# Kernel tuning notes

Hardware: AMD Instinct MI355X
Metric: run time of the kernel (lower is better)

Reference implementation:

```python
import jax, jax.numpy as jnp
import numpy as np

DIM = 512
HEADS = 16
GRID = (32, 32)
MLP_HIDDEN = 2048
EPS = 1e-5


def _relative_position_index(hw):
    H, W = hw
    coords = np.stack(np.meshgrid(np.arange(H), np.arange(W), indexing='ij'))  # [2,H,W]
    coords = coords.reshape(2, -1)  # [2, L]
    rel = coords[:, :, None] - coords[:, None, :]  # [2, L, L]
    rel = rel.transpose(1, 2, 0).astype(np.int64)  # [L, L, 2]
    rel[:, :, 0] += H - 1
    rel[:, :, 1] += W - 1
    rel[:, :, 0] *= 2 * W - 1
    return jnp.asarray(rel.sum(-1))  # [L, L]


def setup_inputs() -> dict:
    key = jax.random.key(0)
    ks = jax.random.split(key, 12)
    L = GRID[0] * GRID[1]
    table_size = (2 * GRID[0] - 1) * (2 * GRID[1] - 1)
    s = 0.02
    return {
        'x': jax.random.normal(ks[0], (8, L, DIM), jnp.float32),
        'rel_index': _relative_position_index(GRID),
        'bias_table': s * jax.random.truncated_normal(ks[1], -2.0, 2.0, (table_size, HEADS), jnp.float32),
        'qkv_w': jax.random.normal(ks[2], (DIM, 3 * DIM), jnp.float32) / np.sqrt(DIM),
        'qkv_b': jnp.zeros((3 * DIM,), jnp.float32),
        'proj_w': jax.random.normal(ks[3], (DIM, DIM), jnp.float32) / np.sqrt(DIM),
        'proj_b': jnp.zeros((DIM,), jnp.float32),
        'n1_g': jnp.ones((DIM,), jnp.float32),
        'n1_b': jnp.zeros((DIM,), jnp.float32),
        'n2_g': jnp.ones((DIM,), jnp.float32),
        'n2_b': jnp.zeros((DIM,), jnp.float32),
        'fc1_w': jax.random.normal(ks[4], (DIM, MLP_HIDDEN), jnp.float32) / np.sqrt(DIM),
        'fc1_b': jnp.zeros((MLP_HIDDEN,), jnp.float32),
        'fc2_w': jax.random.normal(ks[5], (MLP_HIDDEN, DIM), jnp.float32) / np.sqrt(MLP_HIDDEN),
        'fc2_b': jnp.zeros((DIM,), jnp.float32),
    }


def _layernorm(x, g, b):
    mu = jnp.mean(x, -1, keepdims=True)
    var = jnp.mean(jnp.square(x - mu), -1, keepdims=True)
    return (x - mu) * jax.lax.rsqrt(var + EPS) * g + b


def reference(x, rel_index, bias_table, qkv_w, qkv_b, proj_w, proj_b,
              n1_g, n1_b, n2_g, n2_b, fc1_w, fc1_b, fc2_w, fc2_b):
    B, L, C = x.shape
    hd = C // HEADS
    scale = hd ** -0.5

    h = _layernorm(x, n1_g, n1_b)
    qkv = (h @ qkv_w + qkv_b).reshape(B, L, 3, HEADS, hd)
    qkv = jnp.transpose(qkv, (2, 0, 3, 1, 4))  # [3, B, H, L, hd]
    q, k, v = qkv[0] * scale, qkv[1], qkv[2]

    attn = jnp.einsum('bhld,bhmd->bhlm', q, k)  # [B, H, L, L]
    bias = bias_table[rel_index]                # [L, L, H]
    attn = attn + jnp.transpose(bias, (2, 0, 1))[None]
    attn = jax.nn.softmax(attn, axis=-1)

    out = jnp.einsum('bhlm,bhmd->bhld', attn, v)
    out = jnp.transpose(out, (0, 2, 1, 3)).reshape(B, L, C)
    out = out @ proj_w + proj_b

    x = x + out
    h2 = _layernorm(x, n2_g, n2_b)
    mlp = jax.nn.gelu(h2 @ fc1_w + fc1_b, approximate=False) @ fc2_w + fc2_b
    return x + mlp
```

## Files before the change

kernel.cpp:

```cpp
#include <hip/hip_runtime.h>

typedef unsigned short u16;
typedef __attribute__((ext_vector_type(8))) short bf16x8;
typedef __attribute__((ext_vector_type(4))) float f32x4;

__device__ __forceinline__ float bf2f(unsigned int u) {
    union { unsigned int i; float f; } c; c.i = u << 16; return c.f;
}
__device__ __forceinline__ unsigned int f2bf(float f) {
    union { float f; unsigned int i; } c; c.f = f;
    unsigned int x = c.i;
    unsigned int r = x + 0x7FFFu + ((x >> 16) & 1u);
    return r >> 16;
}

__device__ __forceinline__ void gload_lds16(const u16* g, u16* l) {
    __builtin_amdgcn_global_load_lds(
        (__attribute__((address_space(1))) void*)const_cast<u16*>(g),
        (__attribute__((address_space(3))) void*)l,
        16, 0, 0);
}

__global__ __launch_bounds__(256) void wconv_kernel(const float* __restrict__ W,
                                                    u16* __restrict__ Wt, int K, int N) {
    __shared__ u16 tile[32][36];
    int k0 = blockIdx.y * 32, n0 = blockIdx.x * 32;
    int t = threadIdx.x;
    int r = t >> 3, c4 = (t & 7) * 4;
    float4 v = *(const float4*)(W + (size_t)(k0 + r) * N + n0 + c4);
    tile[r][c4 + 0] = (u16)f2bf(v.x);
    tile[r][c4 + 1] = (u16)f2bf(v.y);
    tile[r][c4 + 2] = (u16)f2bf(v.z);
    tile[r][c4 + 3] = (u16)f2bf(v.w);
    __syncthreads();
    int n = t >> 3, k4 = (t & 7) * 4;
    u16 a0 = tile[k4 + 0][n], a1 = tile[k4 + 1][n];
    u16 a2 = tile[k4 + 2][n], a3 = tile[k4 + 3][n];
    uint2 st;
    st.x = (unsigned)a0 | ((unsigned)a1 << 16);
    st.y = (unsigned)a2 | ((unsigned)a3 << 16);
    *(uint2*)(Wt + (size_t)(n0 + n) * K + k0 + k4) = st;
}

__global__ __launch_bounds__(256) void ln_kernel(const float* __restrict__ x,
                                                 const float* __restrict__ g,
                                                 const float* __restrict__ b,
                                                 u16* __restrict__ y) {
    int row = blockIdx.x * 4 + (threadIdx.x >> 6);
    int t = threadIdx.x & 63;
    const float* xr = x + (size_t)row * 512 + t * 8;
    float4 a = *(const float4*)xr;
    float4 c = *(const float4*)(xr + 4);
    float v[8] = { a.x, a.y, a.z, a.w, c.x, c.y, c.z, c.w };
    float s = 0.f, ss = 0.f;
#pragma unroll
    for (int i = 0; i < 8; ++i) { s += v[i]; ss += v[i] * v[i]; }
#pragma unroll
    for (int off = 32; off; off >>= 1) {
        s  += __shfl_down(s, off);
        ss += __shfl_down(ss, off);
    }
    s = __shfl(s, 0); ss = __shfl(ss, 0);
    float mu = s * (1.0f / 512.0f);
    float var = ss * (1.0f / 512.0f) - mu * mu;
    float r = rsqrtf(var + 1e-5f);
    float4 g0 = *(const float4*)(g + t * 8);
    float4 g1 = *(const float4*)(g + t * 8 + 4);
    float4 b0 = *(const float4*)(b + t * 8);
    float4 b1 = *(const float4*)(b + t * 8 + 4);
    float gv[8] = { g0.x, g0.y, g0.z, g0.w, g1.x, g1.y, g1.z, g1.w };
    float bv[8] = { b0.x, b0.y, b0.z, b0.w, b1.x, b1.y, b1.z, b1.w };
    unsigned int o[4];
#pragma unroll
    for (int i = 0; i < 4; ++i) {
        float o0 = (v[2 * i] - mu) * r * gv[2 * i] + bv[2 * i];
        float o1 = (v[2 * i + 1] - mu) * r * gv[2 * i + 1] + bv[2 * i + 1];
        o[i] = f2bf(o0) | (f2bf(o1) << 16);
    }
    *(uint4*)(y + (size_t)row * 512 + t * 8) = make_uint4(o[0], o[1], o[2], o[3]);
}

template <int ACT, int RES, int COUT>
__global__ __launch_bounds__(256) void gemm_mfma(const u16* __restrict__ A, int lda,
                                                 const u16* __restrict__ Bt,
                                                 const float* __restrict__ bias,
                                                 const float* __restrict__ res, int ldres,
                                                 void* __restrict__ C, int ldC, int K) {
    __shared__ u16 As[2][64 * 32];
    __shared__ u16 Bs[2][128 * 32];
    int tid = threadIdx.x;
    int bm = blockIdx.y * 64, bn = blockIdx.x * 128;
    int lane = tid & 63, wv = tid >> 6;
    int q = lane >> 4, lr = lane & 15;
    int wr = wv >> 1, wc = wv & 1;

    const u16* Ag = A + (size_t)(bm + wv * 16 + (lane >> 2)) * lda + (lane & 3) * 8;
    const u16* Bg = Bt + (size_t)(bn + wv * 32 + (lane >> 2)) * K + (lane & 3) * 8;
    int aoff  = (wv * 16) * 32;
    int boff0 = (wv * 32) * 32;
    int boff1 = (wv * 32 + 16) * 32;
    int apf = (wr * 32 + lr) * 32 + q * 8;
    int bpf = (wc * 64 + lr) * 32 + q * 8;

    f32x4 acc[2][4];
#pragma unroll
    for (int i = 0; i < 2; ++i)
#pragma unroll
        for (int j = 0; j < 4; ++j) acc[i][j] = (f32x4){0.f, 0.f, 0.f, 0.f};

    gload_lds16(Ag, &As[0][aoff]);
    gload_lds16(Bg, &Bs[0][boff0]);
    gload_lds16(Bg + (size_t)16 * K, &Bs[0][boff1]);
    __syncthreads();

    int cur = 0;
    for (int k0 = 0; k0 < K; k0 += 32) {
        int nxt = cur ^ 1;
        if (k0 + 32 < K) {
            gload_lds16(Ag + k0 + 32, &As[nxt][aoff]);
            gload_lds16(Bg + k0 + 32, &Bs[nxt][boff0]);
            gload_lds16(Bg + (size_t)16 * K + k0 + 32, &Bs[nxt][boff1]);
        }
        bf16x8 af[2], bfr[4];
#pragma unroll
        for (int i = 0; i < 2; ++i) af[i] = *(const bf16x8*)&As[cur][apf + i * 16 * 32];
#pragma unroll
        for (int j = 0; j < 4; ++j) bfr[j] = *(const bf16x8*)&Bs[cur][bpf + j * 16 * 32];
#pragma unroll
        for (int i = 0; i < 2; ++i)
#pragma unroll
            for (int j = 0; j < 4; ++j)
                acc[i][j] = __builtin_amdgcn_mfma_f32_16x16x32_bf16(af[i], bfr[j], acc[i][j], 0, 0, 0);
        __syncthreads();
        cur = nxt;
    }

    float bv[4];
#pragma unroll
    for (int j = 0; j < 4; ++j)
        bv[j] = bias ? bias[bn + wc * 64 + j * 16 + lr] : 0.f;
#pragma unroll
    for (int i = 0; i < 2; ++i) {
#pragma unroll
        for (int j = 0; j < 4; ++j) {
            int col = bn + wc * 64 + j * 16 + lr;
#pragma unroll
            for (int r = 0; r < 4; ++r) {
                int row = bm + wr * 32 + i * 16 + q * 4 + r;
                float v = acc[i][j][r] + bv[j];
                if (ACT) v = 0.5f * v * (1.0f + erff(v * 0.7071067811865475f));
                if (RES) v += res[(size_t)row * ldres + col];
                if (COUT == 0) ((u16*)C)[(size_t)row * ldC + col] = (u16)f2bf(v);
                else           ((float*)C)[(size_t)row * ldC + col] = v;
            }
        }
    }
}

__global__ __launch_bounds__(256) void attn_mfma(u16* __restrict__ qkv,
                                                 const float* __restrict__ bias_table) {
    __shared__ u16 Ks[128][40];
    __shared__ u16 Vt[32][136];
    __shared__ u16 Ps[4][16][136];
    __shared__ float biasc[3969];
    int tid = threadIdx.x;
    int qt = blockIdx.x, h = blockIdx.y, z = blockIdx.z;
    u16* qkvz = qkv + (size_t)z * 1024 * 1536;

    for (int i = tid; i < 3969; i += 256) biasc[i] = bias_table[(size_t)i * 16 + h];

    int lane = tid & 63, wv = tid >> 6;
    int q = lane >> 4, m = lane & 15;

    int qrow = qt * 64 + wv * 16 + m;
    bf16x8 qf = *(const bf16x8*)(qkvz + (size_t)qrow * 1536 + h * 32 + q * 8);

    int arow[4];
#pragma unroll
    for (int r = 0; r < 4; ++r) {
        int l = qt * 64 + wv * 16 + q * 4 + r;
        arow[r] = (l >> 5) * 63 + (l & 31) + 1984;
    }

    const float scale = 0.17677669529663687f;
    float mrow[4] = { -1e30f, -1e30f, -1e30f, -1e30f };
    float lrow[4] = { 0.f, 0.f, 0.f, 0.f };
    f32x4 acco[2] = { (f32x4){0.f,0.f,0.f,0.f}, (f32x4){0.f,0.f,0.f,0.f} };

    int key = tid >> 1, dh = (tid & 1) * 16;
    const u16* kvsrc = qkvz + (size_t)key * 1536 + 512 + h * 32 + dh;
    uint4 pk0, pk1, pv0, pv1;
    pk0 = *(const uint4*)(kvsrc);
    pk1 = *(const uint4*)(kvsrc + 8);
    pv0 = *(const uint4*)(kvsrc + 512);
    pv1 = *(const uint4*)(kvsrc + 520);

    for (int kt = 0; kt < 8; ++kt) {
        __syncthreads();
        *(uint4*)&Ks[key][dh] = pk0;
        *(uint4*)&Ks[key][dh + 8] = pk1;
        {
            u16 tmp[16];
            *(uint4*)tmp = pv0; *(uint4*)(tmp + 8) = pv1;
#pragma unroll
            for (int j = 0; j < 16; ++j) Vt[dh + j][key] = tmp[j];
        }
        __syncthreads();
        if (kt < 7) {
            const u16* src = kvsrc + (size_t)(kt + 1) * 128 * 1536;
            pk0 = *(const uint4*)(src);
            pk1 = *(const uint4*)(src + 8);
            pv0 = *(const uint4*)(src + 512);
            pv1 = *(const uint4*)(src + 520);
        }

        f32x4 s8[8];
#pragma unroll
        for (int t = 0; t < 8; ++t) {
            bf16x8 kf = *(const bf16x8*)&Ks[t * 16 + m][q * 8];
            s8[t] = __builtin_amdgcn_mfma_f32_16x16x32_bf16(
                qf, kf, (f32x4){0.f,0.f,0.f,0.f}, 0, 0, 0);
        }
#pragma unroll
        for (int t = 0; t < 8; ++t) {
            int bb = (kt * 4 + (t >> 1)) * 63 + (t & 1) * 16 + m;
#pragma unroll
            for (int r = 0; r < 4; ++r)
                s8[t][r] = s8[t][r] * scale + biasc[arow[r] - bb];
        }
        float alpha[4];
#pragma unroll
        for (int r = 0; r < 4; ++r) {
            float v = s8[0][r];
#pragma unroll
            for (int t = 1; t < 8; ++t) v = fmaxf(v, s8[t][r]);
            v = fmaxf(v, __shfl_xor(v, 1));
            v = fmaxf(v, __shfl_xor(v, 2));
            v = fmaxf(v, __shfl_xor(v, 4));
            v = fmaxf(v, __shfl_xor(v, 8));
            float mn = fmaxf(mrow[r], v);
            alpha[r] = __expf(mrow[r] - mn);
            mrow[r] = mn;
            float sum = 0.f;
#pragma unroll
            for (int t = 0; t < 8; ++t) {
                float p = __expf(s8[t][r] - mn);
                s8[t][r] = p;
                sum += p;
            }
            sum += __shfl_xor(sum, 1);
            sum += __shfl_xor(sum, 2);
            sum += __shfl_xor(sum, 4);
            sum += __shfl_xor(sum, 8);
            lrow[r] = lrow[r] * alpha[r] + sum;
        }
#pragma unroll
        for (int t = 0; t < 8; ++t)
#pragma unroll
            for (int r = 0; r < 4; ++r)
                Ps[wv][q * 4 + r][t * 16 + m] = (u16)f2bf(s8[t][r]);
#pragma unroll
        for (int dt = 0; dt < 2; ++dt)
#pragma unroll
            for (int r = 0; r < 4; ++r) acco[dt][r] *= alpha[r];
#pragma unroll
        for (int c = 0; c < 4; ++c) {
            bf16x8 pf = *(const bf16x8*)&Ps[wv][m][c * 32 + q * 8];
#pragma unroll
            for (int dt = 0; dt < 2; ++dt) {
                bf16x8 vf = *(const bf16x8*)&Vt[dt * 16 + m][c * 32 + q * 8];
                acco[dt] = __builtin_amdgcn_mfma_f32_16x16x32_bf16(pf, vf, acco[dt], 0, 0, 0);
            }
        }
    }
#pragma unroll
    for (int r = 0; r < 4; ++r) {
        int l = qt * 64 + wv * 16 + q * 4 + r;
        float inv = 1.0f / lrow[r];
#pragma unroll
        for (int dt = 0; dt < 2; ++dt)
            qkvz[(size_t)l * 1536 + h * 32 + dt * 16 + m] = (u16)f2bf(acco[dt][r] * inv);
    }
}

extern "C" void kernel_launch(void* const* d_in, const int* in_sizes, int n_in,
                              void* d_out, int out_size, void* d_ws, size_t ws_size,
                              hipStream_t stream) {
    const float* x          = (const float*)d_in[0];
    const float* bias_table = (const float*)d_in[2];
    const float* qkv_w      = (const float*)d_in[3];
    const float* qkv_b      = (const float*)d_in[4];
    const float* proj_w     = (const float*)d_in[5];
    const float* proj_b     = (const float*)d_in[6];
    const float* n1g        = (const float*)d_in[7];
    const float* n1b        = (const float*)d_in[8];
    const float* n2g        = (const float*)d_in[9];
    const float* n2b        = (const float*)d_in[10];
    const float* fc1_w      = (const float*)d_in[11];
    const float* fc1_b      = (const float*)d_in[12];
    const float* fc2_w      = (const float*)d_in[13];
    const float* fc2_b      = (const float*)d_in[14];
    float* out = (float*)d_out;

    u16* ws16 = (u16*)d_ws;
    u16* wq_t = ws16;
    u16* wp_t = ws16 + 786432;
    u16* w1_t = ws16 + 1048576;
    u16* w2_t = ws16 + 2097152;
    u16* h    = ws16 + 3145728;
    u16* qkvb = ws16 + 7340032;
    u16* hid  = qkvb;

    wconv_kernel<<<dim3(48, 16), 256, 0, stream>>>(qkv_w, wq_t, 512, 1536);
    wconv_kernel<<<dim3(16, 16), 256, 0, stream>>>(proj_w, wp_t, 512, 512);
    wconv_kernel<<<dim3(64, 16), 256, 0, stream>>>(fc1_w, w1_t, 512, 2048);
    wconv_kernel<<<dim3(16, 64), 256, 0, stream>>>(fc2_w, w2_t, 2048, 512);

    ln_kernel<<<2048, 256, 0, stream>>>(x, n1g, n1b, h);

    for (int half = 0; half < 2; ++half) {
        size_t ro = (size_t)half * 4096;
        gemm_mfma<0, 0, 0><<<dim3(12, 64), 256, 0, stream>>>(
            h + ro * 512, 512, wq_t, qkv_b, nullptr, 0, qkvb, 1536, 512);
        attn_mfma<<<dim3(16, 16, 4), 256, 0, stream>>>(qkvb, bias_table);
        gemm_mfma<0, 1, 1><<<dim3(4, 64), 256, 0, stream>>>(
            qkvb, 1536, wp_t, proj_b, x + ro * 512, 512, out + ro * 512, 512, 512);
    }

    ln_kernel<<<2048, 256, 0, stream>>>(out, n2g, n2b, h);

    for (int half = 0; half < 2; ++half) {
        size_t ro = (size_t)half * 4096;
        gemm_mfma<1, 0, 0><<<dim3(16, 64), 256, 0, stream>>>(
            h + ro * 512, 512, w1_t, fc1_b, nullptr, 0, hid, 2048, 512);
        gemm_mfma<0, 1, 1><<<dim3(4, 64), 256, 0, stream>>>(
            hid, 2048, w2_t, fc2_b, out + ro * 512, 512, out + ro * 512, 512, 2048);
    }
}
```

Measured before the change: 377.4 us.

## Remap blocks across XCDs and double K-step per GEMM iteration

GEMM and attention kernels now use a 1D grid whose block index is remapped so consecutive tiles land on the same XCD (bid&7 striding), improving L2 locality for shared A/B or K/V data. The GEMM main loop also loads two 32-wide K slices per stage (K step 64), halving the number of barriers and making each prefetch larger. LDS use for the GEMM doubles, which may reduce occupancy, and the remap assumes grid sizes divisible by 8.

```diff
diff --git a/kernel.cpp b/kernel.cpp
--- a/kernel.cpp
+++ b/kernel.cpp
@@ -85,11 +85,15 @@
                                                  const u16* __restrict__ Bt,
                                                  const float* __restrict__ bias,
                                                  const float* __restrict__ res, int ldres,
-                                                 void* __restrict__ C, int ldC, int K) {
-    __shared__ u16 As[2][64 * 32];
-    __shared__ u16 Bs[2][128 * 32];
+                                                 void* __restrict__ C, int ldC, int K,
+                                                 int gx) {
+    __shared__ u16 As[2][2][64 * 32];
+    __shared__ u16 Bs[2][2][128 * 32];
     int tid = threadIdx.x;
-    int bm = blockIdx.y * 64, bn = blockIdx.x * 128;
+    int G = gridDim.x;
+    int bid = blockIdx.x;
+    int wg = (bid & 7) * (G >> 3) + (bid >> 3);
+    int bm = (wg / gx) * 64, bn = (wg % gx) * 128;
     int lane = tid & 63, wv = tid >> 6;
     int q = lane >> 4, lr = lane & 15;
     int wr = wv >> 1, wc = wv & 1;
@@ -108,29 +112,38 @@
 #pragma unroll
         for (int j = 0; j < 4; ++j) acc[i][j] = (f32x4){0.f, 0.f, 0.f, 0.f};
 
-    gload_lds16(Ag, &As[0][aoff]);
-    gload_lds16(Bg, &Bs[0][boff0]);
-    gload_lds16(Bg + (size_t)16 * K, &Bs[0][boff1]);
+#pragma unroll
+    for (int p = 0; p < 2; ++p) {
+        gload_lds16(Ag + p * 32, &As[0][p][aoff]);
+        gload_lds16(Bg + p * 32, &Bs[0][p][boff0]);
+        gload_lds16(Bg + (size_t)16 * K + p * 32, &Bs[0][p][boff1]);
+    }
     __syncthreads();
 
     int cur = 0;
-    for (int k0 = 0; k0 < K; k0 += 32) {
+    for (int k0 = 0; k0 < K; k0 += 64) {
         int nxt = cur ^ 1;
-        if (k0 + 32 < K) {
-            gload_lds16(Ag + k0 + 32, &As[nxt][aoff]);
-            gload_lds16(Bg + k0 + 32, &Bs[nxt][boff0]);
-            gload_lds16(Bg + (size_t)16 * K + k0 + 32, &Bs[nxt][boff1]);
-        }
-        bf16x8 af[2], bfr[4];
-#pragma unroll
-        for (int i = 0; i < 2; ++i) af[i] = *(const bf16x8*)&As[cur][apf + i * 16 * 32];
-#pragma unroll
-        for (int j = 0; j < 4; ++j) bfr[j] = *(const bf16x8*)&Bs[cur][bpf + j * 16 * 32];
-#pragma unroll
-        for (int i = 0; i < 2; ++i)
-#pragma unroll
-            for (int j = 0; j < 4; ++j)
-                acc[i][j] = __builtin_amdgcn_mfma_f32_16x16x32_bf16(af[i], bfr[j], acc[i][j], 0, 0, 0);
+        if (k0 + 64 < K) {
+#pragma unroll
+            for (int p = 0; p < 2; ++p) {
+                gload_lds16(Ag + k0 + 64 + p * 32, &As[nxt][p][aoff]);
+                gload_lds16(Bg + k0 + 64 + p * 32, &Bs[nxt][p][boff0]);
+                gload_lds16(Bg + (size_t)16 * K + k0 + 64 + p * 32, &Bs[nxt][p][boff1]);
+            }
+        }
+#pragma unroll
+        for (int p = 0; p < 2; ++p) {
+            bf16x8 af[2], bfr[4];
+#pragma unroll
+            for (int i = 0; i < 2; ++i) af[i] = *(const bf16x8*)&As[cur][p][apf + i * 16 * 32];
+#pragma unroll
+            for (int j = 0; j < 4; ++j) bfr[j] = *(const bf16x8*)&Bs[cur][p][bpf + j * 16 * 32];
+#pragma unroll
+            for (int i = 0; i < 2; ++i)
+#pragma unroll
+                for (int j = 0; j < 4; ++j)
+                    acc[i][j] = __builtin_amdgcn_mfma_f32_16x16x32_bf16(af[i], bfr[j], acc[i][j], 0, 0, 0);
+        }
         __syncthreads();
         cur = nxt;
     }
@@ -164,7 +177,10 @@
     __shared__ u16 Ps[4][16][136];
     __shared__ float biasc[3969];
     int tid = threadIdx.x;
-    int qt = blockIdx.x, h = blockIdx.y, z = blockIdx.z;
+    int bid = blockIdx.x;
+    int grp = (bid & 7) * 8 + ((bid >> 3) >> 4);
+    int qt = (bid >> 3) & 15;
+    int h = grp & 15, z = grp >> 4;
     u16* qkvz = qkv + (size_t)z * 1024 * 1536;
 
     for (int i = tid; i < 3969; i += 256) biasc[i] = bias_table[(size_t)i * 16 + h];
@@ -320,20 +336,20 @@
 
     for (int half = 0; half < 2; ++half) {
         size_t ro = (size_t)half * 4096;
-        gemm_mfma<0, 0, 0><<<dim3(12, 64), 256, 0, stream>>>(
-            h + ro * 512, 512, wq_t, qkv_b, nullptr, 0, qkvb, 1536, 512);
-        attn_mfma<<<dim3(16, 16, 4), 256, 0, stream>>>(qkvb, bias_table);
-        gemm_mfma<0, 1, 1><<<dim3(4, 64), 256, 0, stream>>>(
-            qkvb, 1536, wp_t, proj_b, x + ro * 512, 512, out + ro * 512, 512, 512);
+        gemm_mfma<0, 0, 0><<<dim3(768), 256, 0, stream>>>(
+            h + ro * 512, 512, wq_t, qkv_b, nullptr, 0, qkvb, 1536, 512, 12);
+        attn_mfma<<<dim3(1024), 256, 0, stream>>>(qkvb, bias_table);
+        gemm_mfma<0, 1, 1><<<dim3(256), 256, 0, stream>>>(
+            qkvb, 1536, wp_t, proj_b, x + ro * 512, 512, out + ro * 512, 512, 512, 4);
     }
 
     ln_kernel<<<2048, 256, 0, stream>>>(out, n2g, n2b, h);
 
     for (int half = 0; half < 2; ++half) {
         size_t ro = (size_t)half * 4096;
-        gemm_mfma<1, 0, 0><<<dim3(16, 64), 256, 0, stream>>>(
-            h + ro * 512, 512, w1_t, fc1_b, nullptr, 0, hid, 2048, 512);
-        gemm_mfma<0, 1, 1><<<dim3(4, 64), 256, 0, stream>>>(
-            hid, 2048, w2_t, fc2_b, out + ro * 512, 512, out + ro * 512, 512, 2048);
-    }
-}
+        gemm_mfma<1, 0, 0><<<dim3(1024), 256, 0, stream>>>(
+            h + ro * 512, 512, w1_t, fc1_b, nullptr, 0, hid, 2048, 512, 16);
+        gemm_mfma<0, 1, 1><<<dim3(256), 256, 0, stream>>>(
+            hid, 2048, w2_t, fc2_b, out + ro * 512, 512, out + ro * 512, 512, 2048, 4);
+    }
+}
```

Result: no change. 374.8 us (-0.7%).
